# Performance work log

Measured on AMD Instinct MI355X. Metric: run time of the kernel, lower is better.

The kernel has to match this reference:

```python
import jax, jax.numpy as jnp
import numpy as np

B, S, D = 2, 2048, 1024
H, DH = 16, 64
WINDOW = 256


def setup_inputs() -> dict:
    key = jax.random.key(0)
    ks = jax.random.split(key, 11)
    s = 1.0 / np.sqrt(D)
    return {
        "query": jax.random.normal(ks[0], (B, S, D), jnp.float32),
        "key": jax.random.normal(ks[1], (B, S, D), jnp.float32),
        "value": jax.random.normal(ks[2], (B, S, D), jnp.float32),
        "Wq": jax.random.normal(ks[3], (D, D), jnp.float32) * s,
        "bq": jax.random.normal(ks[4], (D,), jnp.float32) * s,
        "Wk": jax.random.normal(ks[5], (D, D), jnp.float32) * s,
        "bk": jax.random.normal(ks[6], (D,), jnp.float32) * s,
        "Wv": jax.random.normal(ks[7], (D, D), jnp.float32) * s,
        "bv": jax.random.normal(ks[8], (D,), jnp.float32) * s,
        "Wo": jax.random.normal(ks[9], (D, D), jnp.float32) * s,
        "bo": jax.random.normal(ks[10], (D,), jnp.float32) * s,
    }


def reference(query, key, value, Wq, bq, Wk, bk, Wv, bv, Wo, bo):
    scale = DH ** -0.5
    # projections (torch Linear: x @ W.T + b)
    q = query @ Wq.T + bq  # [B,S,D]
    k = key @ Wk.T + bk
    v = value @ Wv.T + bv
    # split heads -> [B,H,S,DH]
    q = q.reshape(B, S, H, DH).transpose(0, 2, 1, 3)
    k = k.reshape(B, S, H, DH).transpose(0, 2, 1, 3)
    v = v.reshape(B, S, H, DH).transpose(0, 2, 1, 3)
    # dense scores with sliding-window causal mask
    attn = jnp.einsum('bhqd,bhkd->bhqk', q, k) * scale  # [B,H,S,S]
    q_idx = jnp.arange(S)[:, None]
    k_idx = jnp.arange(S)[None, :]
    keep = (k_idx <= q_idx) & (k_idx >= q_idx - WINDOW + 1)  # causal & window
    attn = jnp.where(keep[None, None], attn, -jnp.inf)
    attn = jax.nn.softmax(attn, axis=-1)
    # dropout_p=0.0 (eval) -> identity
    out = jnp.einsum('bhqk,bhkd->bhqd', attn, v)  # [B,H,S,DH]
    out = out.transpose(0, 2, 1, 3).reshape(B, S, D)
    return out @ Wo.T + bo
```

## Files before the change

### kernel.cpp

```cpp
#include <hip/hip_runtime.h>
#include <cstdint>
#include <cstddef>

#define B_   2
#define S_   2048
#define D_   1024
#define H_   16
#define DH_  64
#define NROW (B_ * S_)

typedef __bf16  bf16x8 __attribute__((ext_vector_type(8)));
typedef __bf16  bf16x4 __attribute__((ext_vector_type(4)));
typedef float   f32x4  __attribute__((ext_vector_type(4)));

#define MFMA16(a, b, c) __builtin_amdgcn_mfma_f32_16x16x32_bf16((a), (b), (c), 0, 0, 0)

__device__ __forceinline__ void gload_lds16(const void* g, void* l) {
  __builtin_amdgcn_global_load_lds(
      (__attribute__((address_space(1))) void*)(g),
      (__attribute__((address_space(3))) void*)(l), 16, 0, 0);
}

struct CastArgs { const float* src[7]; __bf16* dst[7]; };

__global__ void cast_all(CastArgs a) {
  int b = blockIdx.x, which, idx;
  if (b < 12288) { which = b >> 12; idx = b & 4095; }
  else { b -= 12288; which = 3 + (b >> 10); idx = b & 1023; }
  const int i = idx * 256 + threadIdx.x;
  const float4 v = ((const float4*)a.src[which])[i];
  bf16x4 o;
  o[0] = (__bf16)v.x; o[1] = (__bf16)v.y; o[2] = (__bf16)v.z; o[3] = (__bf16)v.w;
  ((bf16x4*)a.dst[which])[i] = o;
}

struct QKVArgs {
  const __bf16* A[3]; const __bf16* W[3]; const float* bias[3]; __bf16* C[3];
};

__global__ __launch_bounds__(256, 3) void gemm_qkv(QKVArgs args) {
  __shared__ __bf16 As[128 * 64];
  __shared__ __bf16 Bs[128 * 64];
  const int z = blockIdx.z;
  const __bf16* A = args.A[z];
  const __bf16* W = args.W[z];
  const float* bias = args.bias[z];
  __bf16* C = args.C[z];
  const int tid  = threadIdx.x;
  const int lane = tid & 63, wave = tid >> 6;
  const int lo   = lane & 15, quad = lane >> 4;
  const int wr   = wave & 1,  wc   = wave >> 1;
  const int bn   = blockIdx.x, bm = blockIdx.y;
  const __bf16* Ag = A + (size_t)bn * 128 * D_;
  const __bf16* Wg = W + (size_t)bm * 128 * D_;
  int srow[4], soff[4];
#pragma unroll
  for (int u = 0; u < 4; u++) {
    const int c = tid + u * 256;
    srow[u] = c >> 3;
    soff[u] = (((c & 7) ^ ((c >> 3) & 7)) * 8);
  }

  f32x4 acc[4][4] = {};
  for (int k0 = 0; k0 < D_; k0 += 64) {
    __syncthreads();
#pragma unroll
    for (int u = 0; u < 4; u++) {
      gload_lds16(Ag + (size_t)srow[u] * D_ + k0 + soff[u], &As[(tid + u * 256) * 8]);
      gload_lds16(Wg + (size_t)srow[u] * D_ + k0 + soff[u], &Bs[(tid + u * 256) * 8]);
    }
    __syncthreads();
#pragma unroll
    for (int h = 0; h < 2; h++) {
      bf16x8 af[4], bfr[4];
#pragma unroll
      for (int i = 0; i < 4; i++) {
        const int r = wr * 64 + i * 16 + lo;
        af[i] = *(const bf16x8*)&As[r * 64 + (((h * 4 + quad) ^ (r & 7)) * 8)];
      }
#pragma unroll
      for (int j = 0; j < 4; j++) {
        const int r = wc * 64 + j * 16 + lo;
        bfr[j] = *(const bf16x8*)&Bs[r * 64 + (((h * 4 + quad) ^ (r & 7)) * 8)];
      }
#pragma unroll
      for (int i = 0; i < 4; i++)
#pragma unroll
        for (int j = 0; j < 4; j++)
          acc[i][j] = MFMA16(af[i], bfr[j], acc[i][j]);
    }
  }
  if (z == 2) {
#pragma unroll
    for (int i = 0; i < 4; i++) {
      const int row0 = bn * 128 + wr * 64 + i * 16 + quad * 4;
      const int bb = row0 >> 11, s = row0 & (S_ - 1);
#pragma unroll
      for (int j = 0; j < 4; j++) {
        const int col = bm * 128 + wc * 64 + j * 16 + lo;
        const int hh = col >> 6, dd = col & 63;
        const float bv = bias[col];
        bf16x4 o;
#pragma unroll
        for (int r = 0; r < 4; r++) o[r] = (__bf16)(acc[i][j][r] + bv);
        *(bf16x4*)&C[((size_t)(bb * H_ + hh) * DH_ + dd) * S_ + s] = o;
      }
    }
  } else {
#pragma unroll
    for (int i = 0; i < 4; i++) {
      const int row = bn * 128 + wr * 64 + i * 16 + quad * 4;
#pragma unroll
      for (int j = 0; j < 4; j++) {
        const int col = bm * 128 + wc * 64 + j * 16 + lo;
        const float bv = bias[col];
#pragma unroll
        for (int r = 0; r < 4; r++)
          C[(size_t)(row + r) * D_ + col] = (__bf16)(acc[i][j][r] + bv);
      }
    }
  }
}

__global__ __launch_bounds__(256, 3) void attn_win5(
    const __bf16* __restrict__ Qp, const __bf16* __restrict__ Kp,
    const __bf16* __restrict__ Vt, __bf16* __restrict__ ctx) {
  __shared__ __bf16 smem[25600];
  const int qt = blockIdx.x, h = blockIdx.y, b = blockIdx.z;
  const int q0 = qt * 128;
  const int tid = threadIdx.x, wave = tid >> 6, lane = tid & 63;
  const int lo = lane & 15, quad = lane >> 4;
  const int tmin = (q0 >= 256) ? 0 : ((256 - q0) >> 6);
  const __bf16* Kg = Kp + (size_t)b * S_ * D_ + h * DH_;
  const __bf16* Vg = Vt + (size_t)(b * H_ + h) * DH_ * S_;
  const size_t qbase = ((size_t)b * S_) * D_ + h * DH_;

  const int c0 = tid, c1 = tid + 256;
  const int rA = c0 >> 3, gA = ((c0 & 7) ^ (rA & 7)) * 8;
  const int rB = c1 >> 3, gB = ((c1 & 7) ^ (rB & 7)) * 8;

  auto stageK = [&](int t) {
    const int k0 = q0 - 256 + t * 64;
    const int kb = (t & 1) * 4096;
    gload_lds16(Kg + (size_t)(k0 + rA) * D_ + gA, &smem[kb + c0 * 8]);
    gload_lds16(Kg + (size_t)(k0 + rB) * D_ + gB, &smem[kb + c1 * 8]);
  };
  auto stageV = [&](int t) {
    const int k0 = q0 - 256 + t * 64;
    const int vb = 8192 + (t & 1) * 4096;
    gload_lds16(Vg + (size_t)rA * S_ + k0 + gA, &smem[vb + c0 * 8]);
    gload_lds16(Vg + (size_t)rB * S_ + k0 + gB, &smem[vb + c1 * 8]);
  };

  bf16x8 qf[2][2];
#pragma unroll
  for (int f = 0; f < 2; f++) {
    const int qr = q0 + wave * 32 + f * 16 + lo;
    qf[f][0] = *(const bf16x8*)&Qp[qbase + (size_t)qr * D_ + quad * 8];
    qf[f][1] = *(const bf16x8*)&Qp[qbase + (size_t)qr * D_ + 32 + quad * 8];
  }

  stageK(tmin); stageV(tmin);
  stageK(tmin + 1); stageV(tmin + 1);
  __syncthreads();

  const int g0 = (quad ^ (lo & 7)) * 8;
  const int g1 = ((quad + 4) ^ (lo & 7)) * 8;

  const int pwb = 16384 + wave * 2304;
  float rs[2][4] = {};
  f32x4 oacc[2][4] = {};

#pragma unroll
  for (int t = 0; t < 6; t++) {
    if (t < tmin) continue;
    const int kb = (t & 1) * 4096, vb = 8192 + (t & 1) * 4096;
    const int kmin = t * 64 - 256;
    const bool active =
        (kmin <= wave * 32 + 31) && (kmin + 63 > wave * 32 - 256);
    if (active) {
      f32x4 sc[2][4];
#pragma unroll
      for (int kt = 0; kt < 4; kt++) {
        const int kr = kt * 16 + lo;
        const bf16x8 kf0 = *(const bf16x8*)&smem[kb + kr * 64 + g0];
        const bf16x8 kf1 = *(const bf16x8*)&smem[kb + kr * 64 + g1];
#pragma unroll
        for (int f = 0; f < 2; f++) {
          f32x4 c = {0.f, 0.f, 0.f, 0.f};
          c = MFMA16(qf[f][0], kf0, c);
          c = MFMA16(qf[f][1], kf1, c);
          sc[f][kt] = c;
        }
      }
#pragma unroll
      for (int f = 0; f < 2; f++)
#pragma unroll
        for (int kt = 0; kt < 4; kt++)
#pragma unroll
          for (int r = 0; r < 4; r++) {
            const int delta =
                kmin + kt * 16 + lo - (wave * 32 + f * 16 + quad * 4 + r);
            const bool keep = (delta <= 0) && (delta > -256);
            const float e = __expf(fmaf(sc[f][kt][r], 0.125f, -8.0f));
            const float p = keep ? e : 0.0f;
            sc[f][kt][r] = p;
            rs[f][r] += p;
          }
#pragma unroll
      for (int f = 0; f < 2; f++)
#pragma unroll
        for (int kt = 0; kt < 4; kt++)
#pragma unroll
          for (int r = 0; r < 4; r++)
            smem[pwb + (f * 16 + quad * 4 + r) * 72 + kt * 16 + lo] =
                (__bf16)sc[f][kt][r];
      bf16x8 pf[2][2];
#pragma unroll
      for (int f = 0; f < 2; f++) {
        pf[f][0] = *(const bf16x8*)&smem[pwb + (f * 16 + lo) * 72 + quad * 8];
        pf[f][1] = *(const bf16x8*)&smem[pwb + (f * 16 + lo) * 72 + 32 + quad * 8];
      }
#pragma unroll
      for (int ds = 0; ds < 4; ds++) {
        const bf16x8 vf0 = *(const bf16x8*)&smem[vb + (ds * 16 + lo) * 64 + g0];
        const bf16x8 vf1 = *(const bf16x8*)&smem[vb + (ds * 16 + lo) * 64 + g1];
#pragma unroll
        for (int f = 0; f < 2; f++) {
          oacc[f][ds] = MFMA16(pf[f][0], vf0, oacc[f][ds]);
          oacc[f][ds] = MFMA16(pf[f][1], vf1, oacc[f][ds]);
        }
      }
    }
    if (t < 5) {
      __syncthreads();
      if (t + 2 <= 5) { stageK(t + 2); stageV(t + 2); }
    }
  }

#pragma unroll
  for (int f = 0; f < 2; f++)
#pragma unroll
    for (int r = 0; r < 4; r++)
#pragma unroll
      for (int off = 1; off < 16; off <<= 1)
        rs[f][r] += __shfl_xor(rs[f][r], off);

#pragma unroll
  for (int f = 0; f < 2; f++)
#pragma unroll
    for (int ds = 0; ds < 4; ds++)
#pragma unroll
      for (int r = 0; r < 4; r++) {
        const int qg = q0 + wave * 32 + f * 16 + quad * 4 + r;
        ctx[((size_t)b * S_ + qg) * D_ + h * DH_ + ds * 16 + lo] =
            (__bf16)(oacc[f][ds][r] / rs[f][r]);
      }
}

__global__ __launch_bounds__(256, 2) void gemm_o(
    const __bf16* __restrict__ A, const __bf16* __restrict__ W,
    const float* __restrict__ bias, float* __restrict__ C) {
  __shared__ __bf16 As[64 * 64];
  __shared__ __bf16 Bs[128 * 64];
  const int tid = threadIdx.x, lane = tid & 63, wave = tid >> 6;
  const int lo = lane & 15, quad = lane >> 4;
  const int wr = wave & 1, wc = wave >> 1;
  const int bn = blockIdx.x, bm = blockIdx.y;
  const __bf16* Ag = A + (size_t)bn * 64 * D_;
  const __bf16* Wg = W + (size_t)bm * 128 * D_;
  int arow[2], aoff[2], brow[4], boff[4];
#pragma unroll
  for (int u = 0; u < 2; u++) {
    const int c = tid + u * 256;
    arow[u] = c >> 3; aoff[u] = ((c & 7) ^ ((c >> 3) & 7)) * 8;
  }
#pragma unroll
  for (int u = 0; u < 4; u++) {
    const int c = tid + u * 256;
    brow[u] = c >> 3; boff[u] = ((c & 7) ^ ((c >> 3) & 7)) * 8;
  }
  f32x4 acc[2][4] = {};
  for (int k0 = 0; k0 < D_; k0 += 64) {
    __syncthreads();
#pragma unroll
    for (int u = 0; u < 2; u++)
      gload_lds16(Ag + (size_t)arow[u] * D_ + k0 + aoff[u], &As[(tid + u * 256) * 8]);
#pragma unroll
    for (int u = 0; u < 4; u++)
      gload_lds16(Wg + (size_t)brow[u] * D_ + k0 + boff[u], &Bs[(tid + u * 256) * 8]);
    __syncthreads();
#pragma unroll
    for (int h = 0; h < 2; h++) {
      bf16x8 af[2], bfr[4];
#pragma unroll
      for (int i = 0; i < 2; i++) {
        const int r = wr * 32 + i * 16 + lo;
        af[i] = *(const bf16x8*)&As[r * 64 + (((h * 4 + quad) ^ (r & 7)) * 8)];
      }
#pragma unroll
      for (int j = 0; j < 4; j++) {
        const int r = wc * 64 + j * 16 + lo;
        bfr[j] = *(const bf16x8*)&Bs[r * 64 + (((h * 4 + quad) ^ (r & 7)) * 8)];
      }
#pragma unroll
      for (int i = 0; i < 2; i++)
#pragma unroll
        for (int j = 0; j < 4; j++)
          acc[i][j] = MFMA16(af[i], bfr[j], acc[i][j]);
    }
  }
#pragma unroll
  for (int i = 0; i < 2; i++) {
    const int row = bn * 64 + wr * 32 + i * 16 + quad * 4;
#pragma unroll
    for (int j = 0; j < 4; j++) {
      const int col = bm * 128 + wc * 64 + j * 16 + lo;
      const float bv = bias[col];
#pragma unroll
      for (int r = 0; r < 4; r++)
        C[(size_t)(row + r) * D_ + col] = acc[i][j][r] + bv;
    }
  }
}

extern "C" void kernel_launch(void* const* d_in, const int* in_sizes, int n_in,
                              void* d_out, int out_size, void* d_ws, size_t ws_size,
                              hipStream_t stream) {
  (void)in_sizes; (void)n_in; (void)out_size; (void)ws_size;
  const float* q_in = (const float*)d_in[0];
  const float* k_in = (const float*)d_in[1];
  const float* v_in = (const float*)d_in[2];
  const float* Wq   = (const float*)d_in[3];
  const float* bq   = (const float*)d_in[4];
  const float* Wk   = (const float*)d_in[5];
  const float* bk   = (const float*)d_in[6];
  const float* Wv   = (const float*)d_in[7];
  const float* bv   = (const float*)d_in[8];
  const float* Wo   = (const float*)d_in[9];
  const float* bo   = (const float*)d_in[10];

  const size_t XN = (size_t)NROW * D_;
  const size_t WN = (size_t)D_ * D_;
  char* ws = (char*)d_ws;
  __bf16* xq  = (__bf16*)ws; ws += XN * 2;
  __bf16* xk  = (__bf16*)ws; ws += XN * 2;
  __bf16* xv  = (__bf16*)ws; ws += XN * 2;
  __bf16* wqb = (__bf16*)ws; ws += WN * 2;
  __bf16* wkb = (__bf16*)ws; ws += WN * 2;
  __bf16* wvb = (__bf16*)ws; ws += WN * 2;
  __bf16* wob = (__bf16*)ws; ws += WN * 2;
  __bf16* Qp  = (__bf16*)ws; ws += XN * 2;
  __bf16* Kp  = (__bf16*)ws; ws += XN * 2;
  __bf16* Vtp = (__bf16*)ws; ws += XN * 2;
  __bf16* ctx = (__bf16*)ws; ws += XN * 2;

  CastArgs ca;
  ca.src[0] = q_in; ca.src[1] = k_in; ca.src[2] = v_in;
  ca.src[3] = Wq; ca.src[4] = Wk; ca.src[5] = Wv; ca.src[6] = Wo;
  ca.dst[0] = xq; ca.dst[1] = xk; ca.dst[2] = xv;
  ca.dst[3] = wqb; ca.dst[4] = wkb; ca.dst[5] = wvb; ca.dst[6] = wob;
  cast_all<<<16384, 256, 0, stream>>>(ca);

  QKVArgs qa;
  qa.A[0] = xq;  qa.A[1] = xk;  qa.A[2] = xv;
  qa.W[0] = wqb; qa.W[1] = wkb; qa.W[2] = wvb;
  qa.bias[0] = bq; qa.bias[1] = bk; qa.bias[2] = bv;
  qa.C[0] = Qp; qa.C[1] = Kp; qa.C[2] = Vtp;
  gemm_qkv<<<dim3(NROW / 128, D_ / 128, 3), 256, 0, stream>>>(qa);

  attn_win5<<<dim3(S_ / 128, H_, B_), 256, 0, stream>>>(Qp, Kp, Vtp, ctx);

  gemm_o<<<dim3(NROW / 64, D_ / 128), 256, 0, stream>>>(ctx, wob, bo, (float*)d_out);
}
```

Measured before the change: 186.4 us.

## Stage K/V tiles in pairs with four-deep buffering and swizzled P scratch

The attention kernel now loads two 64-key K/V tiles per stage into a four-slot LDS ring, which halves the number of block-wide barriers (three pair iterations instead of six tile iterations). The per-wave probability scratch is shrunk to one 16-row tile with an XOR swizzle that replaces the padded 72-stride layout, reused for each f. LDS use grows to about 72 KB and launch bounds drop to 2 blocks per CU, trading occupancy for fewer syncs. Barrier correctness relies on the ring slots of pair p+2 never overlapping those of pair p+1.

After: 183.4 us. No clear change (-1.6%).

```diff
diff --git a/kernel.cpp b/kernel.cpp
--- a/kernel.cpp
+++ b/kernel.cpp
@@ -122,10 +122,10 @@
   }
 }
 
-__global__ __launch_bounds__(256, 3) void attn_win5(
+__global__ __launch_bounds__(256, 2) void attn_win7(
     const __bf16* __restrict__ Qp, const __bf16* __restrict__ Kp,
     const __bf16* __restrict__ Vt, __bf16* __restrict__ ctx) {
-  __shared__ __bf16 smem[25600];
+  __shared__ __bf16 smem[36864];
   const int qt = blockIdx.x, h = blockIdx.y, b = blockIdx.z;
   const int q0 = qt * 128;
   const int tid = threadIdx.x, wave = tid >> 6, lane = tid & 63;
@@ -141,15 +141,19 @@
 
   auto stageK = [&](int t) {
     const int k0 = q0 - 256 + t * 64;
-    const int kb = (t & 1) * 4096;
+    const int kb = (t & 3) * 4096;
     gload_lds16(Kg + (size_t)(k0 + rA) * D_ + gA, &smem[kb + c0 * 8]);
     gload_lds16(Kg + (size_t)(k0 + rB) * D_ + gB, &smem[kb + c1 * 8]);
   };
   auto stageV = [&](int t) {
     const int k0 = q0 - 256 + t * 64;
-    const int vb = 8192 + (t & 1) * 4096;
+    const int vb = 16384 + (t & 3) * 4096;
     gload_lds16(Vg + (size_t)rA * S_ + k0 + gA, &smem[vb + c0 * 8]);
     gload_lds16(Vg + (size_t)rB * S_ + k0 + gB, &smem[vb + c1 * 8]);
+  };
+  auto stagePair = [&](int p) {
+    stageK(2 * p); stageV(2 * p);
+    stageK(2 * p + 1); stageV(2 * p + 1);
   };
 
   bf16x8 qf[2][2];
@@ -160,81 +164,87 @@
     qf[f][1] = *(const bf16x8*)&Qp[qbase + (size_t)qr * D_ + 32 + quad * 8];
   }
 
-  stageK(tmin); stageV(tmin);
-  stageK(tmin + 1); stageV(tmin + 1);
+  const int p0 = tmin >> 1;
+  stagePair(p0);
+  if (p0 + 1 <= 2) stagePair(p0 + 1);
   __syncthreads();
 
   const int g0 = (quad ^ (lo & 7)) * 8;
   const int g1 = ((quad + 4) ^ (lo & 7)) * 8;
 
-  const int pwb = 16384 + wave * 2304;
+  const int pwb = 32768 + wave * 1024;
   float rs[2][4] = {};
   f32x4 oacc[2][4] = {};
 
 #pragma unroll
-  for (int t = 0; t < 6; t++) {
-    if (t < tmin) continue;
-    const int kb = (t & 1) * 4096, vb = 8192 + (t & 1) * 4096;
-    const int kmin = t * 64 - 256;
-    const bool active =
-        (kmin <= wave * 32 + 31) && (kmin + 63 > wave * 32 - 256);
-    if (active) {
-      f32x4 sc[2][4];
-#pragma unroll
-      for (int kt = 0; kt < 4; kt++) {
-        const int kr = kt * 16 + lo;
-        const bf16x8 kf0 = *(const bf16x8*)&smem[kb + kr * 64 + g0];
-        const bf16x8 kf1 = *(const bf16x8*)&smem[kb + kr * 64 + g1];
+  for (int p = 0; p < 3; p++) {
+    if (p < p0) continue;
+#pragma unroll
+    for (int u = 0; u < 2; u++) {
+      const int t = 2 * p + u;
+      const int kb = (t & 3) * 4096, vb = 16384 + (t & 3) * 4096;
+      const int kmin = t * 64 - 256;
+      const bool active =
+          (kmin <= wave * 32 + 31) && (kmin + 63 > wave * 32 - 256);
+      if (active) {
+        f32x4 sc[2][4];
+#pragma unroll
+        for (int kt = 0; kt < 4; kt++) {
+          const int kr = kt * 16 + lo;
+          const bf16x8 kf0 = *(const bf16x8*)&smem[kb + kr * 64 + g0];
+          const bf16x8 kf1 = *(const bf16x8*)&smem[kb + kr * 64 + g1];
+#pragma unroll
+          for (int f = 0; f < 2; f++) {
+            f32x4 c = {0.f, 0.f, 0.f, 0.f};
+            c = MFMA16(qf[f][0], kf0, c);
+            c = MFMA16(qf[f][1], kf1, c);
+            sc[f][kt] = c;
+          }
+        }
+#pragma unroll
+        for (int f = 0; f < 2; f++)
+#pragma unroll
+          for (int kt = 0; kt < 4; kt++)
+#pragma unroll
+            for (int r = 0; r < 4; r++) {
+              const int delta =
+                  kmin + kt * 16 + lo - (wave * 32 + f * 16 + quad * 4 + r);
+              const bool keep = (delta <= 0) && (delta > -256);
+              const float e = __expf(fmaf(sc[f][kt][r], 0.125f, -8.0f));
+              const float pv = keep ? e : 0.0f;
+              sc[f][kt][r] = pv;
+              rs[f][r] += pv;
+            }
+        bf16x8 pf[2][2];
 #pragma unroll
         for (int f = 0; f < 2; f++) {
-          f32x4 c = {0.f, 0.f, 0.f, 0.f};
-          c = MFMA16(qf[f][0], kf0, c);
-          c = MFMA16(qf[f][1], kf1, c);
-          sc[f][kt] = c;
+#pragma unroll
+          for (int kt = 0; kt < 4; kt++)
+#pragma unroll
+            for (int r = 0; r < 4; r++) {
+              const int row = quad * 4 + r;
+              const int col = kt * 16 + lo;
+              smem[pwb + row * 64 + (((col >> 3) ^ (row & 7)) * 8) + (col & 7)] =
+                  (__bf16)sc[f][kt][r];
+            }
+          pf[f][0] = *(const bf16x8*)&smem[pwb + lo * 64 + g0];
+          pf[f][1] = *(const bf16x8*)&smem[pwb + lo * 64 + g1];
         }
-      }
-#pragma unroll
-      for (int f = 0; f < 2; f++)
-#pragma unroll
-        for (int kt = 0; kt < 4; kt++)
-#pragma unroll
-          for (int r = 0; r < 4; r++) {
-            const int delta =
-                kmin + kt * 16 + lo - (wave * 32 + f * 16 + quad * 4 + r);
-            const bool keep = (delta <= 0) && (delta > -256);
-            const float e = __expf(fmaf(sc[f][kt][r], 0.125f, -8.0f));
-            const float p = keep ? e : 0.0f;
-            sc[f][kt][r] = p;
-            rs[f][r] += p;
+#pragma unroll
+        for (int ds = 0; ds < 4; ds++) {
+          const bf16x8 vf0 = *(const bf16x8*)&smem[vb + (ds * 16 + lo) * 64 + g0];
+          const bf16x8 vf1 = *(const bf16x8*)&smem[vb + (ds * 16 + lo) * 64 + g1];
+#pragma unroll
+          for (int f = 0; f < 2; f++) {
+            oacc[f][ds] = MFMA16(pf[f][0], vf0, oacc[f][ds]);
+            oacc[f][ds] = MFMA16(pf[f][1], vf1, oacc[f][ds]);
           }
-#pragma unroll
-      for (int f = 0; f < 2; f++)
-#pragma unroll
-        for (int kt = 0; kt < 4; kt++)
-#pragma unroll
-          for (int r = 0; r < 4; r++)
-            smem[pwb + (f * 16 + quad * 4 + r) * 72 + kt * 16 + lo] =
-                (__bf16)sc[f][kt][r];
-      bf16x8 pf[2][2];
-#pragma unroll
-      for (int f = 0; f < 2; f++) {
-        pf[f][0] = *(const bf16x8*)&smem[pwb + (f * 16 + lo) * 72 + quad * 8];
-        pf[f][1] = *(const bf16x8*)&smem[pwb + (f * 16 + lo) * 72 + 32 + quad * 8];
-      }
-#pragma unroll
-      for (int ds = 0; ds < 4; ds++) {
-        const bf16x8 vf0 = *(const bf16x8*)&smem[vb + (ds * 16 + lo) * 64 + g0];
-        const bf16x8 vf1 = *(const bf16x8*)&smem[vb + (ds * 16 + lo) * 64 + g1];
-#pragma unroll
-        for (int f = 0; f < 2; f++) {
-          oacc[f][ds] = MFMA16(pf[f][0], vf0, oacc[f][ds]);
-          oacc[f][ds] = MFMA16(pf[f][1], vf1, oacc[f][ds]);
         }
       }
     }
-    if (t < 5) {
+    if (p < 2) {
       __syncthreads();
-      if (t + 2 <= 5) { stageK(t + 2); stageV(t + 2); }
+      if (p + 2 <= 2) stagePair(p + 2);
     }
   }
 
@@ -369,7 +379,7 @@
   qa.C[0] = Qp; qa.C[1] = Kp; qa.C[2] = Vtp;
   gemm_qkv<<<dim3(NROW / 128, D_ / 128, 3), 256, 0, stream>>>(qa);
 
-  attn_win5<<<dim3(S_ / 128, H_, B_), 256, 0, stream>>>(Qp, Kp, Vtp, ctx);
+  attn_win7<<<dim3(S_ / 128, H_, B_), 256, 0, stream>>>(Qp, Kp, Vtp, ctx);
 
   gemm_o<<<dim3(NROW / 64, D_ / 128), 256, 0, stream>>>(ctx, wob, bo, (float*)d_out);
 }
```
